# Performance work log

Measured on AMD Instinct MI355X. Metric: run time of the kernel, lower is better.

Reference implementation:

```python
import jax, jax.numpy as jnp
import numpy as np

IN_FEATURES = 128
OUT_FEATURES = 64
NUM_HEADS = 4
NEGATIVE_SLOPE = 0.2


def setup_inputs() -> dict:
    key = jax.random.key(0)
    k1, k2, k3, k4 = jax.random.split(key, 4)
    B, N = 2, 4096
    inputs = jax.random.normal(k1, (B, N, IN_FEATURES), dtype=jnp.float32)
    # glorot-style scales
    s_w = (6.0 / (IN_FEATURES + OUT_FEATURES * NUM_HEADS)) ** 0.5
    s_a = (6.0 / (OUT_FEATURES + 1)) ** 0.5
    W = jax.random.uniform(k2, (IN_FEATURES, OUT_FEATURES * NUM_HEADS), jnp.float32, -s_w, s_w)
    a_src = jax.random.uniform(k3, (NUM_HEADS, OUT_FEATURES, 1), jnp.float32, -s_a, s_a)
    a_dst = jax.random.uniform(k4, (NUM_HEADS, OUT_FEATURES, 1), jnp.float32, -s_a, s_a)
    bias = jnp.zeros((OUT_FEATURES * NUM_HEADS,), dtype=jnp.float32)
    return {"inputs": inputs, "W": W, "a_src": a_src, "a_dst": a_dst, "bias": bias}


def reference(inputs, W, a_src, a_dst, bias):
    B, N, _ = inputs.shape
    H, D = a_src.shape[0], a_src.shape[1]
    # project and split heads: [B, H, N, D]
    h = jnp.matmul(inputs, W).reshape(B, N, H, D).transpose(0, 2, 1, 3)
    # additive attention scalars per node per head
    e_src = jnp.einsum('bhnd,hd->bhn', h, a_src[..., 0])  # a_src^T (W h_i)
    e_dst = jnp.einsum('bhnd,hd->bhn', h, a_dst[..., 0])  # a_dst^T (W h_j)
    # e[b,h,i,j] = e_src[b,h,i] + e_dst[b,h,j]  (matches e_src + e_dst^T in TF code)
    e = e_src[:, :, :, None] + e_dst[:, :, None, :]
    e = jnp.where(e > 0, e, NEGATIVE_SLOPE * e)  # leaky_relu
    alpha = jax.nn.softmax(e, axis=-1)  # softmax over neighbors j
    # weighted sum of values: [B, H, N, D]
    out = jnp.einsum('bhij,bhjd->bhid', alpha, h)
    out = out.transpose(0, 2, 1, 3).reshape(B, N, H * D)  # concat heads
    out = out + bias
    return jax.nn.elu(out)
```

## Files before the change

### kernel.cpp

```cpp
#include <hip/hip_runtime.h>
#include <hip/hip_fp16.h>
#include <math.h>

#define NH 4
#define DD 64
#define NF 256
#define KF 128
#define NN 4096
#define NB 2
#define NG 8
#define CH 32
#define NCH 128
#define SUB 8

typedef _Float16 h8_t __attribute__((ext_vector_type(8)));
typedef float f4_t __attribute__((ext_vector_type(4)));

__global__ __launch_bounds__(256) void k_gemm(const float* __restrict__ X,
                                              const float* __restrict__ W,
                                              const float* __restrict__ a_src,
                                              const float* __restrict__ a_dst,
                                              __half* __restrict__ Hout,
                                              float* __restrict__ s_arr,
                                              float* __restrict__ d_arr) {
  __shared__ float As[64][132];
  __shared__ _Float16 WT[64][136];
  const int bm = blockIdx.x;
  const int bn = blockIdx.y;
  const int tid = threadIdx.x;

  for (int i = tid; i < 64 * 32; i += 256) {
    int r = i >> 5, c4 = i & 31;
    float4 v = *(const float4*)(X + ((size_t)(bm * 64 + r)) * KF + c4 * 4);
    *(float4*)&As[r][c4 * 4] = v;
  }
  for (int i = tid; i < 64 * 128; i += 256) {
    int k = i >> 6, c = i & 63;
    WT[c][k] = (_Float16)W[(size_t)k * NF + bn * 64 + c];
  }
  __syncthreads();

  const int lane = tid & 63, w = tid >> 6;
  const int l15 = lane & 15, lq = lane >> 4;

  f4_t acc[4] = {f4_t{0.f,0.f,0.f,0.f}, f4_t{0.f,0.f,0.f,0.f},
                 f4_t{0.f,0.f,0.f,0.f}, f4_t{0.f,0.f,0.f,0.f}};

  #pragma unroll
  for (int kk = 0; kk < 4; ++kk) {
    const int koff = kk * 32 + lq * 8;
    h8_t a;
    {
      const float* ap = &As[w * 16 + l15][koff];
      float4 x0 = *(const float4*)ap;
      float4 x1 = *(const float4*)(ap + 4);
      a[0] = (_Float16)x0.x; a[1] = (_Float16)x0.y;
      a[2] = (_Float16)x0.z; a[3] = (_Float16)x0.w;
      a[4] = (_Float16)x1.x; a[5] = (_Float16)x1.y;
      a[6] = (_Float16)x1.z; a[7] = (_Float16)x1.w;
    }
    #pragma unroll
    for (int t = 0; t < 4; ++t) {
      h8_t b = *(const h8_t*)&WT[t * 16 + l15][koff];
      acc[t] = __builtin_amdgcn_mfma_f32_16x16x32_f16(a, b, acc[t], 0, 0, 0);
    }
  }

  float asv[4], adv[4];
  #pragma unroll
  for (int t = 0; t < 4; ++t) {
    asv[t] = a_src[bn * 64 + t * 16 + l15];
    adv[t] = a_dst[bn * 64 + t * 16 + l15];
  }
  #pragma unroll
  for (int j = 0; j < 4; ++j) {
    const int grow = bm * 64 + w * 16 + lq * 4 + j;
    float ps = 0.f, pd = 0.f;
    #pragma unroll
    for (int t = 0; t < 4; ++t) {
      float hv = acc[t][j];
      Hout[(size_t)grow * NF + bn * 64 + t * 16 + l15] = __float2half(hv);
      ps += hv * asv[t];
      pd += hv * adv[t];
    }
    #pragma unroll
    for (int off = 1; off < 16; off <<= 1) {
      ps += __shfl_xor(ps, off);
      pd += __shfl_xor(pd, off);
    }
    if (l15 == 0) {
      int b = grow >> 12, n = grow & (NN - 1);
      int g = b * NH + bn;
      s_arr[g * NN + n] = ps;
      d_arr[g * NN + n] = pd;
    }
  }
}

__global__ __launch_bounds__(512) void k_sort(const float* __restrict__ d_arr,
                                              const float* __restrict__ s_arr,
                                              float* __restrict__ dsort, int* __restrict__ dperm,
                                              float* __restrict__ tsort, int* __restrict__ tperm) {
  __shared__ unsigned skey[8][512];
  __shared__ float vals[NN];
  const int bid = blockIdx.x;
  const bool isT = bid >= NG;
  const int g = isT ? bid - NG : bid;
  const float* src = isT ? s_arr : d_arr;
  float* okey = isT ? tsort : dsort;
  int* operm = isT ? tperm : dperm;
  const int tid = threadIdx.x;

  unsigned kk[8];
  {
    float4 v0 = *(const float4*)(src + g * NN + 8 * tid);
    float4 v1 = *(const float4*)(src + g * NN + 8 * tid + 4);
    float f[8] = {v0.x, v0.y, v0.z, v0.w, v1.x, v1.y, v1.z, v1.w};
    #pragma unroll
    for (int r = 0; r < 8; ++r) {
      float fv = isT ? -f[r] : f[r];
      vals[8 * tid + r] = fv;
      unsigned u = __float_as_uint(fv);
      u = (u & 0x80000000u) ? ~u : (u | 0x80000000u);
      kk[r] = (u & 0xFFFFF000u) | (unsigned)(8 * tid + r);
    }
  }

  #define CEU(a, b, asc)                                           \
    do { unsigned ka = kk[a], kb = kk[b];                          \
      unsigned mn = ka < kb ? ka : kb, mx = ka < kb ? kb : ka;     \
      kk[a] = (asc) ? mn : mx; kk[b] = (asc) ? mx : mn; } while (0)

  CEU(0, 1, true); CEU(2, 3, false); CEU(4, 5, true); CEU(6, 7, false);
  CEU(0, 2, true); CEU(1, 3, true); CEU(4, 6, false); CEU(5, 7, false);
  CEU(0, 1, true); CEU(2, 3, true); CEU(4, 5, false); CEU(6, 7, false);

  #pragma unroll
  for (int k = 8; k <= NN; k <<= 1) {
    const bool asc = (tid & (k >> 3)) == 0;
    #pragma unroll
    for (int j = k >> 1; j > 0; j >>= 1) {
      if (j >= 512) {
        const int tdist = j >> 3;
        #pragma unroll
        for (int r = 0; r < 8; ++r) skey[r][tid] = kk[r];
        __syncthreads();
        const bool keepMin = ((tid & tdist) == 0) == asc;
        #pragma unroll
        for (int r = 0; r < 8; ++r) {
          unsigned pk = skey[r][tid ^ tdist];
          unsigned mn = kk[r] < pk ? kk[r] : pk;
          unsigned mx = kk[r] < pk ? pk : kk[r];
          kk[r] = keepMin ? mn : mx;
        }
        __syncthreads();
      } else if (j >= 8) {
        const int dist = j >> 3;
        const bool keepMin = ((tid & dist) == 0) == asc;
        #pragma unroll
        for (int r = 0; r < 8; ++r) {
          unsigned pk = (unsigned)__shfl_xor((int)kk[r], dist);
          unsigned mn = kk[r] < pk ? kk[r] : pk;
          unsigned mx = kk[r] < pk ? pk : kk[r];
          kk[r] = keepMin ? mn : mx;
        }
      } else if (j == 4) {
        CEU(0, 4, asc); CEU(1, 5, asc); CEU(2, 6, asc); CEU(3, 7, asc);
      } else if (j == 2) {
        CEU(0, 2, asc); CEU(1, 3, asc); CEU(4, 6, asc); CEU(5, 7, asc);
      } else {
        CEU(0, 1, asc); CEU(2, 3, asc); CEU(4, 5, asc); CEU(6, 7, asc);
      }
    }
  }
  #undef CEU

  float ov[8]; int op[8];
  #pragma unroll
  for (int r = 0; r < 8; ++r) {
    int idx = (int)(kk[r] & 0xFFFu);
    ov[r] = vals[idx];
    op[r] = idx;
  }
  *(float4*)(okey + g * NN + 8 * tid)     = make_float4(ov[0], ov[1], ov[2], ov[3]);
  *(float4*)(okey + g * NN + 8 * tid + 4) = make_float4(ov[4], ov[5], ov[6], ov[7]);
  *(int4*)(operm + g * NN + 8 * tid)      = make_int4(op[0], op[1], op[2], op[3]);
  *(int4*)(operm + g * NN + 8 * tid + 4)  = make_int4(op[4], op[5], op[6], op[7]);
}

__global__ __launch_bounds__(256) void k_part(const __half* __restrict__ Hmat,
                                              const float* __restrict__ dsort,
                                              const int* __restrict__ dperm,
                                              float* __restrict__ chunkP, float* __restrict__ chunkS,
                                              float* __restrict__ chunkPw, float* __restrict__ chunkSw) {
  __shared__ float subP[4][64], subS[4][64];
  __shared__ float subPw[4], subSw[4];
  const int ch = blockIdx.x;
  const int g = blockIdx.y;
  const int b = g >> 2, h = g & 3;
  const int c = threadIdx.x & 63;
  const int w = threadIdx.x >> 6;
  const int gNN = g * NN;
  const size_t bNN = (size_t)b * NN;
  const int h64 = h * 64;
  const float dmax = dsort[gNN + NN - 1];
  const int kw0 = ch * CH + w * SUB;

  int j8[SUB]; float d8[SUB], hv8[SUB];
  #pragma unroll
  for (int l = 0; l < SUB; ++l) j8[l] = dperm[gNN + kw0 + l];
  #pragma unroll
  for (int l = 0; l < SUB; ++l) d8[l] = dsort[gNN + kw0 + l];
  #pragma unroll
  for (int l = 0; l < SUB; ++l) hv8[l] = __half2float(Hmat[(bNN + j8[l]) * NF + h64 + c]);

  float pa = 0.f, sa = 0.f, pw = 0.f, sw = 0.f;
  #pragma unroll
  for (int l = 0; l < SUB; ++l) {
    float wp = __expf(0.2f * (d8[l] - dmax));
    float w2 = wp * wp;
    float ws = w2 * w2 * wp;
    pa += wp * hv8[l]; sa += ws * hv8[l]; pw += wp; sw += ws;
  }
  subP[w][c] = pa; subS[w][c] = sa;
  if (c == 0) { subPw[w] = pw; subSw[w] = sw; }
  __syncthreads();

  if (w == 0) {
    float tp = subP[0][c] + subP[1][c] + subP[2][c] + subP[3][c];
    float ts = subS[0][c] + subS[1][c] + subS[2][c] + subS[3][c];
    chunkP[(g * NCH + ch) * 64 + c] = tp;
    chunkS[(g * NCH + ch) * 64 + c] = ts;
    if (c == 0) {
      chunkPw[g * NCH + ch] = subPw[0] + subPw[1] + subPw[2] + subPw[3];
      chunkSw[g * NCH + ch] = subSw[0] + subSw[1] + subSw[2] + subSw[3];
    }
  }
}

__global__ __launch_bounds__(256, 4) void k_serve(const __half* __restrict__ Hmat,
                                                  const float* __restrict__ dsort,
                                                  const int* __restrict__ dperm,
                                                  const float* __restrict__ tsort,
                                                  const int* __restrict__ tperm,
                                                  const float* __restrict__ chunkP, const float* __restrict__ chunkS,
                                                  const float* __restrict__ chunkPw, const float* __restrict__ chunkSw,
                                                  const float* __restrict__ bias,
                                                  float* __restrict__ out) {
  __shared__ float PPloc[CH + 1][64], PSloc[CH + 1][64];
  __shared__ float ppwLoc[CH + 1], pswLoc[CH + 1];
  __shared__ float subP[4][64], subS[4][64], sall[4][64];
  __shared__ float subPw[4], subSw[4];

  const int ch = blockIdx.x & (NCH - 1);
  const int g = blockIdx.x >> 7;
  const int b = g >> 2, h = g & 3;
  const int c = threadIdx.x & 63;
  const int w = threadIdx.x >> 6;
  const int gNN = g * NN;
  const size_t bNN = (size_t)b * NN;
  const int h64 = h * 64;
  const float dmax = dsort[gNN + NN - 1];
  const int kw0 = ch * CH + w * SUB;

  int j8[SUB]; float d8[SUB], hv8[SUB];
  #pragma unroll
  for (int l = 0; l < SUB; ++l) j8[l] = dperm[gNN + kw0 + l];
  #pragma unroll
  for (int l = 0; l < SUB; ++l) d8[l] = dsort[gNN + kw0 + l];
  #pragma unroll
  for (int l = 0; l < SUB; ++l) hv8[l] = __half2float(Hmat[(bNN + j8[l]) * NF + h64 + c]);

  float ppv[SUB], psv[SUB], ppw[SUB], psw[SUB];
  {
    float ap = 0.f, as = 0.f, aw = 0.f, aswv = 0.f;
    #pragma unroll
    for (int l = 0; l < SUB; ++l) {
      float wp = __expf(0.2f * (d8[l] - dmax));
      float w2 = wp * wp;
      float ws = w2 * w2 * wp;
      ap += wp * hv8[l]; as += ws * hv8[l]; aw += wp; aswv += ws;
      ppv[l] = ap; psv[l] = as; ppw[l] = aw; psw[l] = aswv;
    }
    subP[w][c] = ap; subS[w][c] = as;
    if (c == 0) { subPw[w] = aw; subSw[w] = aswv; }
  }
  __syncthreads();

  {
    float oP = 0.f, oS = 0.f, oPw = 0.f, oSw = 0.f;
    #pragma unroll
    for (int t = 0; t < 4; ++t) {
      if (t < w) { oP += subP[t][c]; oS += subS[t][c]; oPw += subPw[t]; oSw += subSw[t]; }
    }
    #pragma unroll
    for (int l = 0; l < SUB; ++l) {
      PPloc[w * SUB + 1 + l][c] = ppv[l] + oP;
      PSloc[w * SUB + 1 + l][c] = psv[l] + oS;
    }
    if (c == 0) {
      #pragma unroll
      for (int l = 0; l < SUB; ++l) {
        ppwLoc[w * SUB + 1 + l] = ppw[l] + oPw;
        pswLoc[w * SUB + 1 + l] = psw[l] + oSw;
      }
    }
    if (w == 0) {
      PPloc[0][c] = 0.f; PSloc[0][c] = 0.f;
      if (c == 0) { ppwLoc[0] = 0.f; pswLoc[0] = 0.f; }
    }
  }
  __syncthreads();

  {
    float pp = 0.f, sp = 0.f, sa = 0.f;
    for (int t = w; t < ch; t += 4) pp += chunkP[(g * NCH + t) * 64 + c];
    for (int t = w; t < NCH; t += 4) {
      float v = chunkS[(g * NCH + t) * 64 + c];
      sa += v;
      if (t < ch) sp += v;
    }
    subP[w][c] = pp; subS[w][c] = sp; sall[w][c] = sa;
  }

  float offPw, offSw, totSw;
  {
    float w1 = chunkPw[g * NCH + c];
    float w2 = chunkPw[g * NCH + 64 + c];
    float pwo = (c < ch ? w1 : 0.f) + (c + 64 < ch ? w2 : 0.f);
    float u1 = chunkSw[g * NCH + c];
    float u2 = chunkSw[g * NCH + 64 + c];
    float swo = (c < ch ? u1 : 0.f) + (c + 64 < ch ? u2 : 0.f);
    float stw = u1 + u2;
    #pragma unroll
    for (int off = 1; off < 64; off <<= 1) {
      pwo += __shfl_xor(pwo, off);
      swo += __shfl_xor(swo, off);
      stw += __shfl_xor(stw, off);
    }
    offPw = pwo; offSw = swo; totSw = stw;
  }
  __syncthreads();

  const float offP = subP[0][c] + subP[1][c] + subP[2][c] + subP[3][c];
  const float offS = subS[0][c] + subS[1][c] + subS[2][c] + subS[3][c];
  const float totS = sall[0][c] + sall[1][c] + sall[2][c] + sall[3][c];

  const float* ts = tsort + gNN;
  int rlo, rhi;
  {
    const float p1 = ts[c * 64 + 63];
    if (ch == 0) rlo = 0;
    else {
      const float blo = dsort[gNN + ch * CH];
      unsigned long long m1 = __ballot(p1 < blo);
      int blk = __popcll(m1);
      if (blk == 64) rlo = NN;
      else {
        float p2 = ts[blk * 64 + c];
        unsigned long long m2 = __ballot(p2 < blo);
        rlo = blk * 64 + __popcll(m2);
      }
    }
    if (ch == NCH - 1) rhi = NN;
    else {
      const float bhi = dsort[gNN + (ch + 1) * CH];
      unsigned long long m1 = __ballot(p1 < bhi);
      int blk = __popcll(m1);
      if (blk == 64) rhi = NN;
      else {
        float p2 = ts[blk * 64 + c];
        unsigned long long m2 = __ballot(p2 < bhi);
        rhi = blk * 64 + __popcll(m2);
      }
    }
  }

  const float myd = (c < 32) ? dsort[gNN + ch * CH + c] : __int_as_float(0x7f800000);
  const float biasv = bias[h64 + c];

  for (int r = rlo + w; r < rhi; r += 4) {
    const float t = ts[r];
    const int i = tperm[gNN + r];
    const int mloc = __popcll(__ballot(myd <= t));
    const float numB = PPloc[mloc][c] + offP;
    const float denB = ppwLoc[mloc] + offPw;
    const float numA = totS - (PSloc[mloc][c] + offS);
    const float denA = totSw - (pswLoc[mloc] + offSw);
    const float si = -t;
    const float sdm = si + dmax;
    const float mx = sdm > 0.f ? sdm : 0.2f * sdm;
    const float alpha = __expf(sdm - mx);
    const float beta = __expf(0.2f * sdm - mx);
    const float den = alpha * denA + beta * denB;
    float val = (alpha * numA + beta * numB) / den + biasv;
    float o = val > 0.f ? val : expm1f(val);
    out[(bNN + i) * NF + h64 + c] = o;
  }
}

extern "C" void kernel_launch(void* const* d_in, const int* in_sizes, int n_in,
                              void* d_out, int out_size, void* d_ws, size_t ws_size,
                              hipStream_t stream) {
  const float* X = (const float*)d_in[0];
  const float* W = (const float*)d_in[1];
  const float* a_src = (const float*)d_in[2];
  const float* a_dst = (const float*)d_in[3];
  const float* bias = (const float*)d_in[4];
  float* out = (float*)d_out;

  float* ws = (float*)d_ws;
  float* s_arr = ws;
  float* d_arr = s_arr + NG * NN;
  float* dsort = d_arr + NG * NN;
  int* dperm = (int*)(dsort + NG * NN);
  float* tsort = (float*)(dperm + NG * NN);
  int* tperm = (int*)(tsort + NG * NN);
  float* chunkP = (float*)(tperm + NG * NN);
  float* chunkS = chunkP + NG * NCH * 64;
  float* chunkPw = chunkS + NG * NCH * 64;
  float* chunkSw = chunkPw + NG * NCH;
  __half* Hmat = (__half*)(chunkSw + NG * NCH);

  k_gemm<<<dim3(128, 4), 256, 0, stream>>>(X, W, a_src, a_dst, Hmat, s_arr, d_arr);
  k_sort<<<2 * NG, 512, 0, stream>>>(d_arr, s_arr, dsort, dperm, tsort, tperm);
  k_part<<<dim3(NCH, NG), 256, 0, stream>>>(Hmat, dsort, dperm, chunkP, chunkS, chunkPw, chunkSw);
  k_serve<<<NG * NCH, 256, 0, stream>>>(Hmat, dsort, dperm, tsort, tperm,
                                        chunkP, chunkS, chunkPw, chunkSw, bias, out);
}
```

Baseline: 57.68 us.

## Precompute chunk prefix tables in k_part and load them in k_serve

k_part now computes the per-chunk inclusive prefix sums of weighted values and weights and writes them to new global tables. k_serve no longer gathers Hmat rows or recomputes exponentials. It copies the precomputed table into shared memory instead. This removes duplicated gather and exp work from the serve kernel. In exchange it adds a large global write and read of the prefix tables, and the workspace grows.

```diff
diff --git a/kernel.cpp b/kernel.cpp
--- a/kernel.cpp
+++ b/kernel.cpp
@@ -12,6 +12,7 @@
 #define CH 32
 #define NCH 128
 #define SUB 8
+#define TE 33
 
 typedef _Float16 h8_t __attribute__((ext_vector_type(8)));
 typedef float f4_t __attribute__((ext_vector_type(4)));
@@ -192,7 +193,9 @@
                                               const float* __restrict__ dsort,
                                               const int* __restrict__ dperm,
                                               float* __restrict__ chunkP, float* __restrict__ chunkS,
-                                              float* __restrict__ chunkPw, float* __restrict__ chunkSw) {
+                                              float* __restrict__ chunkPw, float* __restrict__ chunkSw,
+                                              float* __restrict__ PPtab, float* __restrict__ PStab,
+                                              float* __restrict__ pwTab, float* __restrict__ swTab) {
   __shared__ float subP[4][64], subS[4][64];
   __shared__ float subPw[4], subSw[4];
   const int ch = blockIdx.x;
@@ -214,19 +217,45 @@
   #pragma unroll
   for (int l = 0; l < SUB; ++l) hv8[l] = __half2float(Hmat[(bNN + j8[l]) * NF + h64 + c]);
 
-  float pa = 0.f, sa = 0.f, pw = 0.f, sw = 0.f;
+  float ppv[SUB], psv[SUB], ppw[SUB], psw[SUB];
+  {
+    float ap = 0.f, as = 0.f, aw = 0.f, aswv = 0.f;
+    #pragma unroll
+    for (int l = 0; l < SUB; ++l) {
+      float wp = __expf(0.2f * (d8[l] - dmax));
+      float w2 = wp * wp;
+      float ws = w2 * w2 * wp;
+      ap += wp * hv8[l]; as += ws * hv8[l]; aw += wp; aswv += ws;
+      ppv[l] = ap; psv[l] = as; ppw[l] = aw; psw[l] = aswv;
+    }
+    subP[w][c] = ap; subS[w][c] = as;
+    if (c == 0) { subPw[w] = aw; subSw[w] = aswv; }
+  }
+  __syncthreads();
+
+  float oP = 0.f, oS = 0.f, oPw = 0.f, oSw = 0.f;
+  #pragma unroll
+  for (int t = 0; t < 4; ++t) {
+    if (t < w) { oP += subP[t][c]; oS += subS[t][c]; oPw += subPw[t]; oSw += subSw[t]; }
+  }
+
+  const size_t tb = (size_t)(g * NCH + ch) * TE;
   #pragma unroll
   for (int l = 0; l < SUB; ++l) {
-    float wp = __expf(0.2f * (d8[l] - dmax));
-    float w2 = wp * wp;
-    float ws = w2 * w2 * wp;
-    pa += wp * hv8[l]; sa += ws * hv8[l]; pw += wp; sw += ws;
-  }
-  subP[w][c] = pa; subS[w][c] = sa;
-  if (c == 0) { subPw[w] = pw; subSw[w] = sw; }
-  __syncthreads();
-
+    PPtab[(tb + w * SUB + 1 + l) * 64 + c] = ppv[l] + oP;
+    PStab[(tb + w * SUB + 1 + l) * 64 + c] = psv[l] + oS;
+  }
+  if (c == 0) {
+    #pragma unroll
+    for (int l = 0; l < SUB; ++l) {
+      pwTab[tb + w * SUB + 1 + l] = ppw[l] + oPw;
+      swTab[tb + w * SUB + 1 + l] = psw[l] + oSw;
+    }
+  }
   if (w == 0) {
+    PPtab[tb * 64 + c] = 0.f;
+    PStab[tb * 64 + c] = 0.f;
+    if (c == 0) { pwTab[tb] = 0.f; swTab[tb] = 0.f; }
     float tp = subP[0][c] + subP[1][c] + subP[2][c] + subP[3][c];
     float ts = subS[0][c] + subS[1][c] + subS[2][c] + subS[3][c];
     chunkP[(g * NCH + ch) * 64 + c] = tp;
@@ -238,79 +267,42 @@
   }
 }
 
-__global__ __launch_bounds__(256, 4) void k_serve(const __half* __restrict__ Hmat,
-                                                  const float* __restrict__ dsort,
-                                                  const int* __restrict__ dperm,
+__global__ __launch_bounds__(256, 4) void k_serve(const float* __restrict__ dsort,
                                                   const float* __restrict__ tsort,
                                                   const int* __restrict__ tperm,
                                                   const float* __restrict__ chunkP, const float* __restrict__ chunkS,
                                                   const float* __restrict__ chunkPw, const float* __restrict__ chunkSw,
+                                                  const float* __restrict__ PPtab, const float* __restrict__ PStab,
+                                                  const float* __restrict__ pwTab, const float* __restrict__ swTab,
                                                   const float* __restrict__ bias,
                                                   float* __restrict__ out) {
-  __shared__ float PPloc[CH + 1][64], PSloc[CH + 1][64];
-  __shared__ float ppwLoc[CH + 1], pswLoc[CH + 1];
+  __shared__ float PPloc[TE][64], PSloc[TE][64];
+  __shared__ float ppwLoc[TE], pswLoc[TE];
   __shared__ float subP[4][64], subS[4][64], sall[4][64];
-  __shared__ float subPw[4], subSw[4];
 
   const int ch = blockIdx.x & (NCH - 1);
   const int g = blockIdx.x >> 7;
   const int b = g >> 2, h = g & 3;
   const int c = threadIdx.x & 63;
   const int w = threadIdx.x >> 6;
+  const int tid = threadIdx.x;
   const int gNN = g * NN;
   const size_t bNN = (size_t)b * NN;
   const int h64 = h * 64;
   const float dmax = dsort[gNN + NN - 1];
-  const int kw0 = ch * CH + w * SUB;
-
-  int j8[SUB]; float d8[SUB], hv8[SUB];
-  #pragma unroll
-  for (int l = 0; l < SUB; ++l) j8[l] = dperm[gNN + kw0 + l];
-  #pragma unroll
-  for (int l = 0; l < SUB; ++l) d8[l] = dsort[gNN + kw0 + l];
-  #pragma unroll
-  for (int l = 0; l < SUB; ++l) hv8[l] = __half2float(Hmat[(bNN + j8[l]) * NF + h64 + c]);
-
-  float ppv[SUB], psv[SUB], ppw[SUB], psw[SUB];
-  {
-    float ap = 0.f, as = 0.f, aw = 0.f, aswv = 0.f;
-    #pragma unroll
-    for (int l = 0; l < SUB; ++l) {
-      float wp = __expf(0.2f * (d8[l] - dmax));
-      float w2 = wp * wp;
-      float ws = w2 * w2 * wp;
-      ap += wp * hv8[l]; as += ws * hv8[l]; aw += wp; aswv += ws;
-      ppv[l] = ap; psv[l] = as; ppw[l] = aw; psw[l] = aswv;
-    }
-    subP[w][c] = ap; subS[w][c] = as;
-    if (c == 0) { subPw[w] = aw; subSw[w] = aswv; }
-  }
-  __syncthreads();
-
-  {
-    float oP = 0.f, oS = 0.f, oPw = 0.f, oSw = 0.f;
-    #pragma unroll
-    for (int t = 0; t < 4; ++t) {
-      if (t < w) { oP += subP[t][c]; oS += subS[t][c]; oPw += subPw[t]; oSw += subSw[t]; }
-    }
-    #pragma unroll
-    for (int l = 0; l < SUB; ++l) {
-      PPloc[w * SUB + 1 + l][c] = ppv[l] + oP;
-      PSloc[w * SUB + 1 + l][c] = psv[l] + oS;
-    }
-    if (c == 0) {
-      #pragma unroll
-      for (int l = 0; l < SUB; ++l) {
-        ppwLoc[w * SUB + 1 + l] = ppw[l] + oPw;
-        pswLoc[w * SUB + 1 + l] = psw[l] + oSw;
-      }
-    }
-    if (w == 0) {
-      PPloc[0][c] = 0.f; PSloc[0][c] = 0.f;
-      if (c == 0) { ppwLoc[0] = 0.f; pswLoc[0] = 0.f; }
-    }
-  }
-  __syncthreads();
+
+  {
+    const size_t tb = (size_t)(g * NCH + ch) * TE;
+    const float4* srcP = (const float4*)(PPtab + tb * 64);
+    const float4* srcS = (const float4*)(PStab + tb * 64);
+    float4* dstP = (float4*)&PPloc[0][0];
+    float4* dstS = (float4*)&PSloc[0][0];
+    for (int i = tid; i < TE * 16; i += 256) { dstP[i] = srcP[i]; dstS[i] = srcS[i]; }
+    if (tid < TE) {
+      ppwLoc[tid] = pwTab[tb + tid];
+      pswLoc[tid] = swTab[tb + tid];
+    }
+  }
 
   {
     float pp = 0.f, sp = 0.f, sa = 0.f;
@@ -420,11 +412,17 @@
   float* chunkS = chunkP + NG * NCH * 64;
   float* chunkPw = chunkS + NG * NCH * 64;
   float* chunkSw = chunkPw + NG * NCH;
-  __half* Hmat = (__half*)(chunkSw + NG * NCH);
+  float* PPtab = chunkSw + NG * NCH;
+  float* PStab = PPtab + (size_t)NG * NCH * TE * 64;
+  float* pwTab = PStab + (size_t)NG * NCH * TE * 64;
+  float* swTab = pwTab + (size_t)NG * NCH * TE;
+  __half* Hmat = (__half*)(swTab + (size_t)NG * NCH * TE);
 
   k_gemm<<<dim3(128, 4), 256, 0, stream>>>(X, W, a_src, a_dst, Hmat, s_arr, d_arr);
   k_sort<<<2 * NG, 512, 0, stream>>>(d_arr, s_arr, dsort, dperm, tsort, tperm);
-  k_part<<<dim3(NCH, NG), 256, 0, stream>>>(Hmat, dsort, dperm, chunkP, chunkS, chunkPw, chunkSw);
-  k_serve<<<NG * NCH, 256, 0, stream>>>(Hmat, dsort, dperm, tsort, tperm,
-                                        chunkP, chunkS, chunkPw, chunkSw, bias, out);
+  k_part<<<dim3(NCH, NG), 256, 0, stream>>>(Hmat, dsort, dperm, chunkP, chunkS, chunkPw, chunkSw,
+                                            PPtab, PStab, pwTab, swTab);
+  k_serve<<<NG * NCH, 256, 0, stream>>>(dsort, tsort, tperm,
+                                        chunkP, chunkS, chunkPw, chunkSw,
+                                        PPtab, PStab, pwTab, swTab, bias, out);
 }
```

After: 62.12 us. 7.7% more time.
